# Optimization experiments

Hardware: AMD Instinct MI355X
Metric: run time of the kernel (lower is better)

## Reference

```python
import jax, jax.numpy as jnp
import numpy as np

ALPHA = 0.01  # leakyrelu negative slope


def setup_inputs() -> dict:
    key = jax.random.key(0)
    k1, k2, k3 = jax.random.split(key, 3)
    B, N, F_in, F_out = 32, 1024, 256, 256
    inp = jax.random.normal(k1, (B, N, F_in), dtype=jnp.float32)
    # xavier_uniform-like scale, gain=1.414
    lim_W = 1.414 * np.sqrt(6.0 / (F_in + F_out))
    W = jax.random.uniform(k2, (F_in, F_out), dtype=jnp.float32, minval=-lim_W, maxval=lim_W)
    lim_a = 1.414 * np.sqrt(6.0 / (2 * F_out + 1))
    a = jax.random.uniform(k3, (2 * F_out, 1), dtype=jnp.float32, minval=-lim_a, maxval=lim_a)
    return {"inp": inp, "W": W, "a": a}


def reference(inp, W, a):
    # h: [B, N, F_out]
    h = jnp.matmul(inp, W)
    F_out = W.shape[1]
    # Additive attention: score[b,i,j] = leakyrelu(h[b,i]@a1 + h[b,j]@a2).
    # Mathematically identical to cat([h_i, h_j]) @ a without materializing
    # the O(N^2 * 2F) a_input tensor.
    a1 = a[:F_out, 0]  # [F_out]
    a2 = a[F_out:, 0]  # [F_out]
    f1 = jnp.einsum('bnf,f->bn', h, a1)  # [B, N]
    f2 = jnp.einsum('bnf,f->bn', h, a2)  # [B, N]
    e = f1[:, :, None] + f2[:, None, :]  # [B, N, N]
    e = jnp.where(e > 0, e, ALPHA * e)   # leakyrelu
    attention = jax.nn.softmax(e, axis=-1)
    # dropout omitted (deterministic eval-mode reference)
    h_prime = jnp.matmul(attention, h)   # [B, N, F_out]
    return jax.nn.elu(h_prime)
```

## Files before the change

kernel.cpp:

```cpp
#include <hip/hip_runtime.h>
#include <hip/hip_bf16.h>

typedef unsigned short u16;
typedef unsigned int u32;
typedef __attribute__((ext_vector_type(4))) float f32x4;
typedef __attribute__((ext_vector_type(8))) _Float16 f16x8;
typedef __attribute__((ext_vector_type(8))) unsigned short u16x8;

#define LRELU(x) ((x) > 0.f ? (x) : 0.01f * (x))

static __device__ __forceinline__ u16 f2h(float x) {
    _Float16 h = (_Float16)x;
    u16 r;
    __builtin_memcpy(&r, &h, 2);
    return r;
}
static __device__ __forceinline__ float h2f(u16 v) {
    _Float16 h;
    __builtin_memcpy(&h, &v, 2);
    return (float)h;
}

__global__ void k_prep(const float* __restrict__ W, const float* __restrict__ a,
                       u16* __restrict__ Wt_hi, u16* __restrict__ Wt_lo,
                       float* __restrict__ w1, float* __restrict__ w2) {
    int i = blockIdx.x, t = threadIdx.x;
    float x = W[i * 256 + t];
    float p1 = x * a[t];
    float p2 = x * a[256 + t];
#pragma unroll
    for (int off = 1; off < 64; off <<= 1) {
        p1 += __shfl_xor(p1, off);
        p2 += __shfl_xor(p2, off);
    }
    __shared__ float s1[4], s2[4];
    if ((t & 63) == 0) { s1[t >> 6] = p1; s2[t >> 6] = p2; }
    __syncthreads();
    if (t == 0) {
        w1[i] = s1[0] + s1[1] + s1[2] + s1[3];
        w2[i] = s2[0] + s2[1] + s2[2] + s2[3];
    }
    float y = W[t * 256 + i];
    u16 hi = f2h(y);
    Wt_hi[i * 256 + t] = hi;
    Wt_lo[i * 256 + t] = f2h(y - h2f(hi));
}

__global__ void k_m(const float* __restrict__ f2, float* __restrict__ Mb) {
    int b = blockIdx.x, t = threadIdx.x;
    float m = -1e30f;
#pragma unroll
    for (int j = 0; j < 4; ++j) m = fmaxf(m, f2[b * 1024 + t + j * 256]);
#pragma unroll
    for (int off = 1; off < 64; off <<= 1) m = fmaxf(m, __shfl_xor(m, off));
    __shared__ float s[4];
    if ((t & 63) == 0) s[t >> 6] = m;
    __syncthreads();
    if (t == 0) Mb[b] = fmaxf(fmaxf(s[0], s[1]), fmaxf(s[2], s[3]));
}

__global__ __launch_bounds__(256, 4) void k_h(const float* __restrict__ inp,
                                              const u16* __restrict__ Wt_hi,
                                              const u16* __restrict__ Wt_lo,
                                              const float* __restrict__ w1,
                                              const float* __restrict__ w2,
                                              u16* __restrict__ ht,
                                              float* __restrict__ f1,
                                              float* __restrict__ f2) {
    __shared__ float sw1[256], sw2[256];
    int t = threadIdx.x, w = t >> 6, l = t & 63, lr = l & 15, lk = l >> 4;
    sw1[t] = w1[t];
    sw2[t] = w2[t];
    __syncthreads();
    int n0 = blockIdx.x * 32;
    int bb = n0 >> 10, nb0 = n0 & 1023;

    f32x4 acc[4][2];
#pragma unroll
    for (int i = 0; i < 4; ++i)
#pragma unroll
        for (int j = 0; j < 2; ++j)
#pragma unroll
            for (int r = 0; r < 4; ++r) acc[i][j][r] = 0.f;
    float d1[2] = {0.f, 0.f}, d2[2] = {0.f, 0.f};

    for (int kt = 0; kt < 8; ++kt) {
        int k0 = kt * 32 + lk * 8;
        f16x8 ah[4], al[4];
#pragma unroll
        for (int it = 0; it < 4; ++it) {
            int f = w * 64 + it * 16 + lr;
            ah[it] = *(const f16x8*)&Wt_hi[f * 256 + k0];
            al[it] = *(const f16x8*)&Wt_lo[f * 256 + k0];
        }
        f32x4 c1a = *(const f32x4*)&sw1[k0];
        f32x4 c1b = *(const f32x4*)&sw1[k0 + 4];
        f32x4 c2a = *(const f32x4*)&sw2[k0];
        f32x4 c2b = *(const f32x4*)&sw2[k0 + 4];
#pragma unroll
        for (int ci = 0; ci < 2; ++ci) {
            int n = n0 + ci * 16 + lr;
            f32x4 v0 = *(const f32x4*)&inp[n * 256 + k0];
            f32x4 v1 = *(const f32x4*)&inp[n * 256 + k0 + 4];
            d1[ci] += v0.x * c1a.x + v0.y * c1a.y + v0.z * c1a.z + v0.w * c1a.w +
                      v1.x * c1b.x + v1.y * c1b.y + v1.z * c1b.z + v1.w * c1b.w;
            d2[ci] += v0.x * c2a.x + v0.y * c2a.y + v0.z * c2a.z + v0.w * c2a.w +
                      v1.x * c2b.x + v1.y * c2b.y + v1.z * c2b.z + v1.w * c2b.w;
            u16x8 hv, lv;
#pragma unroll
            for (int j = 0; j < 4; ++j) {
                u16 h0 = f2h(v0[j]);
                hv[j] = h0;
                lv[j] = f2h(v0[j] - h2f(h0));
                u16 h1 = f2h(v1[j]);
                hv[j + 4] = h1;
                lv[j + 4] = f2h(v1[j] - h2f(h1));
            }
            f16x8 bh = *(f16x8*)&hv, bl = *(f16x8*)&lv;
#pragma unroll
            for (int it = 0; it < 4; ++it) {
                acc[it][ci] = __builtin_amdgcn_mfma_f32_16x16x32_f16(ah[it], bh, acc[it][ci], 0, 0, 0);
                acc[it][ci] = __builtin_amdgcn_mfma_f32_16x16x32_f16(ah[it], bl, acc[it][ci], 0, 0, 0);
                acc[it][ci] = __builtin_amdgcn_mfma_f32_16x16x32_f16(al[it], bh, acc[it][ci], 0, 0, 0);
            }
        }
    }
#pragma unroll
    for (int ci = 0; ci < 2; ++ci) {
        d1[ci] += __shfl_xor(d1[ci], 16);
        d1[ci] += __shfl_xor(d1[ci], 32);
        d2[ci] += __shfl_xor(d2[ci], 16);
        d2[ci] += __shfl_xor(d2[ci], 32);
    }
    if (w == 0 && l < 16) {
#pragma unroll
        for (int ci = 0; ci < 2; ++ci) {
            f1[n0 + ci * 16 + l] = d1[ci];
            f2[n0 + ci * 16 + l] = d2[ci];
        }
    }
#pragma unroll
    for (int it = 0; it < 4; ++it)
#pragma unroll
        for (int ci = 0; ci < 2; ++ci) {
            int col = nb0 + ci * 16 + lr;
#pragma unroll
            for (int r = 0; r < 4; ++r) {
                int F = w * 64 + it * 16 + lk * 4 + r;
                ht[(size_t)(bb * 256 + F) * 1024 + col] = f2h(acc[it][ci][r]);
            }
        }
}

__global__ __launch_bounds__(256, 4) void k_attn(const u16* __restrict__ ht,
                                                 const float* __restrict__ f1,
                                                 const float* __restrict__ f2,
                                                 const float* __restrict__ Mb,
                                                 float* __restrict__ out) {
    __shared__ float sf2[1024];
    __shared__ u16 P[2][2][4][512];
    __shared__ float rs[64];
    int t = threadIdx.x, w = t >> 6, l = t & 63, lr = l & 15, lk = l >> 4;
    int g = blockIdx.x;
    int xcd = g & 7, idx = g >> 3;
    int b = xcd * 4 + (idx >> 5);
    int i0 = (idx & 31) * 32;

    *(f32x4*)&sf2[t * 4] = *(const f32x4*)&f2[b * 1024 + t * 4];
    float Mv = Mb[b];
    int rgp = w & 1;
    int jh = w >> 1;
    float f1v = f1[b * 1024 + i0 + rgp * 16 + lr];
    float miv = LRELU(f1v + Mv);
    float lsum = 0.f;
    const u16* H = ht + (size_t)b * 262144;

    auto computeP = [&](int cc2, int buf2) {
#pragma unroll
        for (int ss = 0; ss < 2; ++ss) {
            int s = jh * 2 + ss;
            int jb = cc2 * 128 + s * 32 + lk * 8;
            f32x4 fa = *(const f32x4*)&sf2[jb];
            f32x4 fb = *(const f32x4*)&sf2[jb + 4];
            u16x8 pv;
#pragma unroll
            for (int jj = 0; jj < 8; ++jj) {
                float fv = (jj < 4) ? fa[jj] : fb[jj - 4];
                float e = LRELU(f1v + fv);
                float p = __expf(e - miv);
                lsum += p;
                pv[jj] = f2h(p);
            }
            *(u16x8*)&P[buf2][rgp][s][l * 8] = pv;
        }
    };

    f32x4 acc[2][4];
#pragma unroll
    for (int i = 0; i < 2; ++i)
#pragma unroll
        for (int j = 0; j < 4; ++j)
#pragma unroll
            for (int r = 0; r < 4; ++r) acc[i][j][r] = 0.f;

    __syncthreads();
    computeP(0, 0);

    for (int cc = 0; cc < 8; ++cc) {
        __syncthreads();
        if (cc < 7) computeP(cc + 1, (cc + 1) & 1);
        int buf = cc & 1;
#pragma unroll
        for (int s = 0; s < 4; ++s) {
            int jcol = cc * 128 + s * 32 + lk * 8;
            f16x8 pf0 = *(const f16x8*)&P[buf][0][s][l * 8];
            f16x8 pf1 = *(const f16x8*)&P[buf][1][s][l * 8];
            __builtin_amdgcn_s_setprio(1);
#pragma unroll
            for (int ci = 0; ci < 4; ++ci) {
                int f = w * 64 + ci * 16 + lr;
                f16x8 bh = *(const f16x8*)&H[(size_t)f * 1024 + jcol];
                acc[0][ci] = __builtin_amdgcn_mfma_f32_16x16x32_f16(pf0, bh, acc[0][ci], 0, 0, 0);
                acc[1][ci] = __builtin_amdgcn_mfma_f32_16x16x32_f16(pf1, bh, acc[1][ci], 0, 0, 0);
            }
            __builtin_amdgcn_s_setprio(0);
        }
    }

    lsum += __shfl_xor(lsum, 16);
    lsum += __shfl_xor(lsum, 32);
    if (l < 16) rs[w * 16 + lr] = lsum;
    __syncthreads();

#pragma unroll
    for (int it = 0; it < 2; ++it) {
        f32x4 s1 = *(const f32x4*)&rs[it * 16 + lk * 4];
        f32x4 s2 = *(const f32x4*)&rs[(it + 2) * 16 + lk * 4];
        f32x4 sums = s1 + s2;
#pragma unroll
        for (int ci = 0; ci < 4; ++ci) {
            int col = w * 64 + ci * 16 + lr;
            int rowg = b * 1024 + i0 + it * 16 + lk * 4;
#pragma unroll
            for (int r = 0; r < 4; ++r) {
                float v = acc[it][ci][r] / sums[r];
                v = v > 0.f ? v : (__expf(v) - 1.f);
                out[(size_t)(rowg + r) * 256 + col] = v;
            }
        }
    }
}

extern "C" void kernel_launch(void* const* d_in, const int* in_sizes, int n_in,
                              void* d_out, int out_size, void* d_ws, size_t ws_size,
                              hipStream_t stream) {
    const float* inp = (const float*)d_in[0];
    const float* W = (const float*)d_in[1];
    const float* a = (const float*)d_in[2];
    float* out = (float*)d_out;

    char* ws = (char*)d_ws;
    u16* ht = (u16*)(ws + 0);
    u16* Wt_hi = (u16*)(ws + 16777216);
    u16* Wt_lo = (u16*)(ws + 16908288);
    float* w1 = (float*)(ws + 17039360);
    float* w2 = (float*)(ws + 17040384);
    float* f1 = (float*)(ws + 17041408);
    float* f2 = (float*)(ws + 17172480);
    float* Mb = (float*)(ws + 17303552);

    k_prep<<<256, 256, 0, stream>>>(W, a, Wt_hi, Wt_lo, w1, w2);
    k_h<<<1024, 256, 0, stream>>>(inp, Wt_hi, Wt_lo, w1, w2, ht, f1, f2);
    k_m<<<32, 256, 0, stream>>>(f2, Mb);
    k_attn<<<1024, 256, 0, stream>>>(ht, f1, f2, Mb, out);
}
```

Before: 201.2 us.

## Compute softmax probabilities per wave in registers, drop LDS staging and barriers

Each wave now computes the full 32x64 probability tile it needs for the MFMA A operand directly in registers, instead of splitting the work across waves and exchanging it through double-buffered LDS with a __syncthreads each chunk. f2 is read straight from global memory, H loads for a 64-column step are issued before the exp work, exp is done with exp2 and a prescaled max, and conversion uses packed RTZ. Row sums are reduced with shuffles, which removes all shared memory and block barriers. In exchange, each wave does four times the exp/ALU work (every wave recomputes the same P), and register pressure rises.

```diff
diff --git a/kernel.cpp b/kernel.cpp
--- a/kernel.cpp
+++ b/kernel.cpp
@@ -5,6 +5,7 @@
 typedef unsigned int u32;
 typedef __attribute__((ext_vector_type(4))) float f32x4;
 typedef __attribute__((ext_vector_type(8))) _Float16 f16x8;
+typedef __attribute__((ext_vector_type(2))) __fp16 hp16x2;
 typedef __attribute__((ext_vector_type(8))) unsigned short u16x8;
 
 #define LRELU(x) ((x) > 0.f ? (x) : 0.01f * (x))
@@ -157,44 +158,22 @@
                                                  const float* __restrict__ f2,
                                                  const float* __restrict__ Mb,
                                                  float* __restrict__ out) {
-    __shared__ float sf2[1024];
-    __shared__ u16 P[2][2][4][512];
-    __shared__ float rs[64];
     int t = threadIdx.x, w = t >> 6, l = t & 63, lr = l & 15, lk = l >> 4;
     int g = blockIdx.x;
     int xcd = g & 7, idx = g >> 3;
     int b = xcd * 4 + (idx >> 5);
     int i0 = (idx & 31) * 32;
 
-    *(f32x4*)&sf2[t * 4] = *(const f32x4*)&f2[b * 1024 + t * 4];
+    const float L2E = 1.44269504f;
+    const float* F2 = f2 + b * 1024;
     float Mv = Mb[b];
-    int rgp = w & 1;
-    int jh = w >> 1;
-    float f1v = f1[b * 1024 + i0 + rgp * 16 + lr];
-    float miv = LRELU(f1v + Mv);
-    float lsum = 0.f;
+    float f1v0 = f1[b * 1024 + i0 + lr];
+    float f1v1 = f1[b * 1024 + i0 + 16 + lr];
+    float mb0 = LRELU(f1v0 + Mv) * L2E;
+    float mb1 = LRELU(f1v1 + Mv) * L2E;
+    float ls0 = 0.f, ls1 = 0.f;
     const u16* H = ht + (size_t)b * 262144;
 
-    auto computeP = [&](int cc2, int buf2) {
-#pragma unroll
-        for (int ss = 0; ss < 2; ++ss) {
-            int s = jh * 2 + ss;
-            int jb = cc2 * 128 + s * 32 + lk * 8;
-            f32x4 fa = *(const f32x4*)&sf2[jb];
-            f32x4 fb = *(const f32x4*)&sf2[jb + 4];
-            u16x8 pv;
-#pragma unroll
-            for (int jj = 0; jj < 8; ++jj) {
-                float fv = (jj < 4) ? fa[jj] : fb[jj - 4];
-                float e = LRELU(f1v + fv);
-                float p = __expf(e - miv);
-                lsum += p;
-                pv[jj] = f2h(p);
-            }
-            *(u16x8*)&P[buf2][rgp][s][l * 8] = pv;
-        }
-    };
-
     f32x4 acc[2][4];
 #pragma unroll
     for (int i = 0; i < 2; ++i)
@@ -203,40 +182,74 @@
 #pragma unroll
             for (int r = 0; r < 4; ++r) acc[i][j][r] = 0.f;
 
-    __syncthreads();
-    computeP(0, 0);
-
-    for (int cc = 0; cc < 8; ++cc) {
-        __syncthreads();
-        if (cc < 7) computeP(cc + 1, (cc + 1) & 1);
-        int buf = cc & 1;
-#pragma unroll
-        for (int s = 0; s < 4; ++s) {
-            int jcol = cc * 128 + s * 32 + lk * 8;
-            f16x8 pf0 = *(const f16x8*)&P[buf][0][s][l * 8];
-            f16x8 pf1 = *(const f16x8*)&P[buf][1][s][l * 8];
-            __builtin_amdgcn_s_setprio(1);
-#pragma unroll
-            for (int ci = 0; ci < 4; ++ci) {
-                int f = w * 64 + ci * 16 + lr;
-                f16x8 bh = *(const f16x8*)&H[(size_t)f * 1024 + jcol];
-                acc[0][ci] = __builtin_amdgcn_mfma_f32_16x16x32_f16(pf0, bh, acc[0][ci], 0, 0, 0);
-                acc[1][ci] = __builtin_amdgcn_mfma_f32_16x16x32_f16(pf1, bh, acc[1][ci], 0, 0, 0);
-            }
-            __builtin_amdgcn_s_setprio(0);
-        }
-    }
-
-    lsum += __shfl_xor(lsum, 16);
-    lsum += __shfl_xor(lsum, 32);
-    if (l < 16) rs[w * 16 + lr] = lsum;
-    __syncthreads();
+    for (int jt = 0; jt < 16; ++jt) {
+        int jc0 = jt * 64 + lk * 8;
+        int jc1 = jc0 + 32;
+        f16x8 bh0[4], bh1[4];
+#pragma unroll
+        for (int ci = 0; ci < 4; ++ci) {
+            const u16* Hp = H + (size_t)(w * 64 + ci * 16 + lr) * 1024;
+            bh0[ci] = *(const f16x8*)&Hp[jc0];
+            bh1[ci] = *(const f16x8*)&Hp[jc1];
+        }
+        f32x4 fa0 = *(const f32x4*)&F2[jc0];
+        f32x4 fb0 = *(const f32x4*)&F2[jc0 + 4];
+        f32x4 fa1 = *(const f32x4*)&F2[jc1];
+        f32x4 fb1 = *(const f32x4*)&F2[jc1 + 4];
+        union { f16x8 v; hp16x2 h[4]; } p00, p01, p10, p11;
+        float pt0[8], pt1[8];
+#pragma unroll
+        for (int jj = 0; jj < 8; ++jj) {
+            float fv = (jj < 4) ? fa0[jj] : fb0[jj - 4];
+            float e0 = f1v0 + fv, e1 = f1v1 + fv;
+            e0 = fmaxf(e0, 0.01f * e0);
+            e1 = fmaxf(e1, 0.01f * e1);
+            float q0 = __builtin_amdgcn_exp2f(fmaf(e0, L2E, -mb0));
+            float q1 = __builtin_amdgcn_exp2f(fmaf(e1, L2E, -mb1));
+            ls0 += q0; ls1 += q1;
+            pt0[jj] = q0; pt1[jj] = q1;
+        }
+#pragma unroll
+        for (int jj = 0; jj < 4; ++jj) {
+            p00.h[jj] = __builtin_amdgcn_cvt_pkrtz(pt0[2 * jj], pt0[2 * jj + 1]);
+            p10.h[jj] = __builtin_amdgcn_cvt_pkrtz(pt1[2 * jj], pt1[2 * jj + 1]);
+        }
+#pragma unroll
+        for (int jj = 0; jj < 8; ++jj) {
+            float fv = (jj < 4) ? fa1[jj] : fb1[jj - 4];
+            float e0 = f1v0 + fv, e1 = f1v1 + fv;
+            e0 = fmaxf(e0, 0.01f * e0);
+            e1 = fmaxf(e1, 0.01f * e1);
+            float q0 = __builtin_amdgcn_exp2f(fmaf(e0, L2E, -mb0));
+            float q1 = __builtin_amdgcn_exp2f(fmaf(e1, L2E, -mb1));
+            ls0 += q0; ls1 += q1;
+            pt0[jj] = q0; pt1[jj] = q1;
+        }
+#pragma unroll
+        for (int jj = 0; jj < 4; ++jj) {
+            p01.h[jj] = __builtin_amdgcn_cvt_pkrtz(pt0[2 * jj], pt0[2 * jj + 1]);
+            p11.h[jj] = __builtin_amdgcn_cvt_pkrtz(pt1[2 * jj], pt1[2 * jj + 1]);
+        }
+#pragma unroll
+        for (int ci = 0; ci < 4; ++ci) {
+            acc[0][ci] = __builtin_amdgcn_mfma_f32_16x16x32_f16(p00.v, bh0[ci], acc[0][ci], 0, 0, 0);
+            acc[1][ci] = __builtin_amdgcn_mfma_f32_16x16x32_f16(p10.v, bh0[ci], acc[1][ci], 0, 0, 0);
+            acc[0][ci] = __builtin_amdgcn_mfma_f32_16x16x32_f16(p01.v, bh1[ci], acc[0][ci], 0, 0, 0);
+            acc[1][ci] = __builtin_amdgcn_mfma_f32_16x16x32_f16(p11.v, bh1[ci], acc[1][ci], 0, 0, 0);
+        }
+    }
+
+    ls0 += __shfl_xor(ls0, 16);
+    ls0 += __shfl_xor(ls0, 32);
+    ls1 += __shfl_xor(ls1, 16);
+    ls1 += __shfl_xor(ls1, 32);
 
 #pragma unroll
     for (int it = 0; it < 2; ++it) {
-        f32x4 s1 = *(const f32x4*)&rs[it * 16 + lk * 4];
-        f32x4 s2 = *(const f32x4*)&rs[(it + 2) * 16 + lk * 4];
-        f32x4 sums = s1 + s2;
+        float lsv = (it == 0) ? ls0 : ls1;
+        float sums[4];
+#pragma unroll
+        for (int r = 0; r < 4; ++r) sums[r] = __shfl(lsv, lk * 4 + r);
 #pragma unroll
         for (int ci = 0; ci < 4; ++ci) {
             int col = w * 64 + ci * 16 + lr;
```

Result: slower. 206.8 us (+2.8%).
